# Optimization experiments

Hardware: AMD Instinct MI355X
Metric: run time of the kernel (lower is better)

The kernel has to match this reference:

```python
import jax, jax.numpy as jnp
import numpy as np

B, S, EMB, H = 4, 1024, 1024, 16
HD = EMB // H          # head_dim = 64
MAXP = 512             # RelativePositionalEncoder default max_position


def setup_inputs() -> dict:
    key = jax.random.key(0)
    ks = jax.random.split(key, 13)
    s = 1.0 / np.sqrt(EMB)  # xavier-ish scale keeps softmax logits sane
    return {
        "query": jax.random.normal(ks[0], (B, S, EMB), jnp.float32),
        "key": jax.random.normal(ks[1], (B, S, EMB), jnp.float32),
        "value": jax.random.normal(ks[2], (B, S, EMB), jnp.float32),
        "Wq": jax.random.normal(ks[3], (EMB, EMB), jnp.float32) * s,
        "bq": jnp.zeros((EMB,), jnp.float32),
        "Wk": jax.random.normal(ks[4], (EMB, EMB), jnp.float32) * s,
        "bk": jnp.zeros((EMB,), jnp.float32),
        "Wv": jax.random.normal(ks[5], (EMB, EMB), jnp.float32) * s,
        "bv": jnp.zeros((EMB,), jnp.float32),
        "Wo": jax.random.normal(ks[6], (EMB, EMB), jnp.float32) * s,
        "bo": jnp.zeros((EMB,), jnp.float32),
        "rel_k": jax.random.normal(ks[7], (2 * MAXP + 1, HD), jnp.float32) * 0.05,
        "rel_v": jax.random.normal(ks[8], (2 * MAXP + 1, HD), jnp.float32) * 0.05,
    }


def _split_heads(x):
    # [B,S,E] -> [B,S,H,HD] -> [B,H,S,HD] -> [B*H,S,HD]
    return x.reshape(B, S, H, HD).transpose(0, 2, 1, 3).reshape(B * H, S, HD)


def reference(query, key, value, Wq, bq, Wk, bk, Wv, bv, Wo, bo, rel_k, rel_v):
    scale = jnp.sqrt(jnp.asarray(HD, query.dtype))
    q = _split_heads(query @ Wq + bq)
    k = _split_heads(key @ Wk + bk)
    v = _split_heads(value @ Wv + bv)
    # relative position lookup tables: [Sq, Sk, HD]
    rp = jnp.clip(jnp.arange(S)[None, :] - jnp.arange(S)[:, None], -MAXP, MAXP) + MAXP
    a_key = rel_k[rp]
    a_value = rel_v[rp]
    qk = jnp.einsum('bqd,bkd->bqk', q, k)              # [B*H,S,S]
    rel_qk = jnp.einsum('bqd,qkd->bqk', q, a_key)      # relative score term
    attn = jax.nn.softmax((qk + rel_qk) / scale, axis=-1)
    out = jnp.einsum('bqk,bkd->bqd', attn, v) + jnp.einsum('bqk,qkd->bqd', attn, a_value)
    # faithful to original's view(num_heads, batch, -1, head_dim) then concat reshape
    out = out.reshape(H, B, S, HD).transpose(0, 2, 1, 3).reshape(B, S, H * HD)
    out = out @ Wo + bo
    return (out, attn)
```

## Files before the change

### kernel.cpp

```cpp
#include <hip/hip_runtime.h>


using s16x8 = __attribute__((ext_vector_type(8))) short;
using f32x4 = __attribute__((ext_vector_type(4))) float;

#define MFMA16 __builtin_amdgcn_mfma_f32_16x16x32_bf16

__device__ __forceinline__ float bf2f(unsigned short u) {
  union { unsigned int u; float f; } v; v.u = ((unsigned int)u) << 16; return v.f;
}
__device__ __forceinline__ unsigned short f2bf(float f) {
  union { float f; unsigned int u; } v; v.f = f;
  unsigned int r = (v.u + 0x7FFFu + ((v.u >> 16) & 1u)) >> 16;
  return (unsigned short)r;
}

__global__ void k_cvt_bf16(const float* __restrict__ in, unsigned short* __restrict__ out, int n) {
  int i = (blockIdx.x * 256 + threadIdx.x) * 8;
  if (i >= n) return;
  float4 a = *(const float4*)(in + i);
  float4 b = *(const float4*)(in + i + 4);
  s16x8 o;
  o[0] = (short)f2bf(a.x); o[1] = (short)f2bf(a.y); o[2] = (short)f2bf(a.z); o[3] = (short)f2bf(a.w);
  o[4] = (short)f2bf(b.x); o[5] = (short)f2bf(b.y); o[6] = (short)f2bf(b.z); o[7] = (short)f2bf(b.w);
  *(s16x8*)(out + i) = o;
}

__global__ void k_tr1024(const float* __restrict__ W, unsigned short* __restrict__ Wt) {
  __shared__ float t[32][33];
  int tx = threadIdx.x, ty = threadIdx.y;
  int n0 = blockIdx.x * 32, k0 = blockIdx.y * 32;
#pragma unroll
  for (int r = 0; r < 4; ++r)
    t[ty * 4 + r][tx] = W[(size_t)(k0 + ty * 4 + r) * 1024 + n0 + tx];
  __syncthreads();
#pragma unroll
  for (int r = 0; r < 4; ++r)
    Wt[(size_t)(n0 + ty * 4 + r) * 1024 + k0 + tx] = f2bf(t[tx][ty * 4 + r]);
}

__global__ void k_relprep(const float* __restrict__ rk, const float* __restrict__ rv,
                          unsigned short* __restrict__ relkb, unsigned short* __restrict__ rvTb) {
  int b = blockIdx.x;
  if (b < 33) {
    int i = (b * 256 + threadIdx.x) * 8;
    if (i < 65600) {
      float4 a = *(const float4*)(rk + i);
      float4 c = *(const float4*)(rk + i + 4);
      s16x8 o;
      o[0] = (short)f2bf(a.x); o[1] = (short)f2bf(a.y); o[2] = (short)f2bf(a.z); o[3] = (short)f2bf(a.w);
      o[4] = (short)f2bf(c.x); o[5] = (short)f2bf(c.y); o[6] = (short)f2bf(c.z); o[7] = (short)f2bf(c.w);
      *(s16x8*)(relkb + i) = o;
    }
  } else {
    int i = (b - 33) * 256 + threadIdx.x;
    if (i < 65600) {
      int p = i >> 6, d = i & 63;
      rvTb[d * 1040 + p] = f2bf(rv[i]);
    }
  }
}

__global__ __launch_bounds__(256)
void k_trV(const unsigned short* __restrict__ v, unsigned short* __restrict__ vt) {
  __shared__ unsigned short T[64][72];
  const int tid = threadIdx.x;
  const int bh = blockIdx.x >> 4;
  const int s0 = (blockIdx.x & 15) << 6;
  const int r = tid >> 2, cb = (tid & 3) << 4;
  const unsigned short* src = v + ((size_t)bh << 16) + (size_t)(s0 + r) * 64 + cb;
  *(s16x8*)&T[r][cb] = *(const s16x8*)src;
  *(s16x8*)&T[r][cb + 8] = *(const s16x8*)(src + 8);
  __syncthreads();
  unsigned short* dst = vt + ((size_t)bh << 16) + (size_t)r * 1024 + s0 + cb;
  s16x8 o0, o1;
#pragma unroll
  for (int e = 0; e < 8; ++e) o0[e] = T[cb + e][r];
#pragma unroll
  for (int e = 0; e < 8; ++e) o1[e] = T[cb + 8 + e][r];
  *(s16x8*)dst = o0;
  *(s16x8*)(dst + 8) = o1;
}

template <int MODE>
__global__ __launch_bounds__(256, 2)
void k_gemm(const unsigned short* __restrict__ A, const unsigned short* __restrict__ BT,
            const float* __restrict__ bias, void* __restrict__ Cout) {
  __shared__ alignas(16) unsigned short aT[2][4096];
  __shared__ alignas(16) unsigned short bT[2][4096];
  const int tid = threadIdx.x;
  const int lane = tid & 63;
  const int l15 = lane & 15, lhi = lane >> 4;
  const int w = tid >> 6;
  const int wr = (w >> 1) * 64, wc = (w & 1) * 64;
  const int brow = blockIdx.y * 128, bcol = blockIdx.x * 128;
  f32x4 acc[4][4] = {};

#define STAGE(buf, kt) do {                                                              \
    int k0s = (kt) * 32;                                                                 \
    {                                                                                    \
      int c = tid;                                                                       \
      int row = c >> 2, k8 = (c & 3) * 8;                                                \
      __builtin_amdgcn_global_load_lds(                                                  \
        (const __attribute__((address_space(1))) void*)(A + (size_t)(brow + row) * 1024 + k0s + k8), \
        (__attribute__((address_space(3))) void*)(&aT[buf][c * 8]), 16, 0, 0);           \
      __builtin_amdgcn_global_load_lds(                                                  \
        (const __attribute__((address_space(1))) void*)(BT + (size_t)(bcol + row) * 1024 + k0s + k8),\
        (__attribute__((address_space(3))) void*)(&bT[buf][c * 8]), 16, 0, 0);           \
    }                                                                                    \
    {                                                                                    \
      int c = tid + 256;                                                                 \
      int row = c >> 2, k8 = (c & 3) * 8;                                                \
      __builtin_amdgcn_global_load_lds(                                                  \
        (const __attribute__((address_space(1))) void*)(A + (size_t)(brow + row) * 1024 + k0s + k8), \
        (__attribute__((address_space(3))) void*)(&aT[buf][c * 8]), 16, 0, 0);           \
      __builtin_amdgcn_global_load_lds(                                                  \
        (const __attribute__((address_space(1))) void*)(BT + (size_t)(bcol + row) * 1024 + k0s + k8),\
        (__attribute__((address_space(3))) void*)(&bT[buf][c * 8]), 16, 0, 0);           \
    }                                                                                    \
  } while (0)

  int cur = 0;
  STAGE(0, 0);
  for (int kt = 0; kt < 32; ++kt) {
    __syncthreads();
    if (kt + 1 < 32) STAGE(cur ^ 1, kt + 1);
    s16x8 af[4], bfv[4];
#pragma unroll
    for (int m = 0; m < 4; ++m)
      af[m] = *(const s16x8*)&aT[cur][(wr + m * 16 + l15) * 32 + lhi * 8];
#pragma unroll
    for (int n = 0; n < 4; ++n)
      bfv[n] = *(const s16x8*)&bT[cur][(wc + n * 16 + l15) * 32 + lhi * 8];
#pragma unroll
    for (int m = 0; m < 4; ++m)
#pragma unroll
      for (int n = 0; n < 4; ++n)
        acc[m][n] = MFMA16(af[m], bfv[n], acc[m][n], 0, 0, 0);
    __syncthreads();
    cur ^= 1;
  }
#undef STAGE

#pragma unroll
  for (int m = 0; m < 4; ++m) {
#pragma unroll
    for (int n = 0; n < 4; ++n) {
      int col = bcol + wc + n * 16 + l15;
      float bs = bias[col];
#pragma unroll
      for (int j = 0; j < 4; ++j) {
        int r = brow + wr + m * 16 + lhi * 4 + j;
        float v = acc[m][n][j] + bs;
        if (MODE == 0) {
          int b = r >> 10, s = r & 1023, h = col >> 6, d = col & 63;
          ((unsigned short*)Cout)[(((size_t)((b << 4) + h) * 1024 + s) << 6) + d] = f2bf(v);
        } else {
          ((float*)Cout)[(size_t)r * 1024 + col] = v;
        }
      }
    }
  }
}

#define RPW 1032
#define PWP 520

__global__ __launch_bounds__(256, 3)
void k_attn(const unsigned short* __restrict__ qb, const unsigned short* __restrict__ kbm,
            const unsigned short* __restrict__ vT, const unsigned short* __restrict__ relk,
            const unsigned short* __restrict__ rvT, float* __restrict__ attn_out,
            unsigned short* __restrict__ xscr) {
  __shared__ alignas(16) unsigned short pbuf[16 * RPW];
  __shared__ alignas(16) unsigned short pw[16 * PWP];
  __shared__ float red[3][4][16];
  __shared__ float izS[16], plS[16], phS[16];

  const int tid = threadIdx.x;
  const int lane = tid & 63;
  const int w = tid >> 6;
  const int l15 = lane & 15, lhi = lane >> 4;
  const int bh = blockIdx.x >> 6;
  const int q0 = (blockIdx.x & 63) << 4;

  const unsigned short* Qh = qb + ((size_t)bh << 16);
  const unsigned short* Kh = kbm + ((size_t)bh << 16);
  const unsigned short* Vth = vT + ((size_t)bh << 16);

  const unsigned short* qp = Qh + (size_t)(q0 + l15) * 64 + lhi * 8;
  s16x8 qa0 = *(const s16x8*)qp;
  s16x8 qa1 = *(const s16x8*)(qp + 32);

  float zp[4] = {0.f, 0.f, 0.f, 0.f};
  float lo[4] = {0.f, 0.f, 0.f, 0.f};
  float hi4[4] = {0.f, 0.f, 0.f, 0.f};
  for (int k0 = w * 16; k0 < 1024; k0 += 64) {
    const unsigned short* kp = Kh + (size_t)(k0 + l15) * 64 + lhi * 8;
    s16x8 kf0 = *(const s16x8*)kp;
    s16x8 kf1 = *(const s16x8*)(kp + 32);
    const int jb = k0 - q0 - 15;
    int p0 = jb + l15;      p0 = (p0 < -512 ? -512 : (p0 > 512 ? 512 : p0)) + 512;
    int p1 = jb + l15 + 16; p1 = (p1 < -512 ? -512 : (p1 > 512 ? 512 : p1)) + 512;
    const unsigned short* r0p = relk + (size_t)p0 * 64 + lhi * 8;
    const unsigned short* r1p = relk + (size_t)p1 * 64 + lhi * 8;
    s16x8 ra0 = *(const s16x8*)r0p, ra0h = *(const s16x8*)(r0p + 32);
    s16x8 ra1 = *(const s16x8*)r1p, ra1h = *(const s16x8*)(r1p + 32);
    f32x4 c = {0.f, 0.f, 0.f, 0.f};
    f32x4 w0 = {0.f, 0.f, 0.f, 0.f}, w1 = {0.f, 0.f, 0.f, 0.f};
    __builtin_amdgcn_s_setprio(1);
    c = MFMA16(qa0, kf0, c, 0, 0, 0);
    c = MFMA16(qa1, kf1, c, 0, 0, 0);
    w0 = MFMA16(qa0, ra0, w0, 0, 0, 0);  w0 = MFMA16(qa1, ra0h, w0, 0, 0, 0);
    w1 = MFMA16(qa0, ra1, w1, 0, 0, 0);  w1 = MFMA16(qa1, ra1h, w1, 0, 0, 0);
    __builtin_amdgcn_s_setprio(0);
#pragma unroll
    for (int j = 0; j < 4; ++j) {
      int qi = lhi * 4 + j;
      int ts = l15 - qi + 15;
      int sl = (lane & 48) | (ts & 15);
      float a0 = __shfl(w0[j], sl, 64);
      float a1 = __shfl(w1[j], sl, 64);
      float rel = (ts & 16) ? a1 : a0;
      float e = __expf((c[j] + rel) * 0.125f);
      zp[j] += e;
      int dd = k0 + l15 - q0 - qi;
      lo[j]  += (dd <= -512) ? e : 0.f;
      hi4[j] += (dd >=  512) ? e : 0.f;
      pbuf[qi * RPW + k0 + l15] = f2bf(e);
    }
  }
#pragma unroll
  for (int off = 1; off < 16; off <<= 1)
#pragma unroll
    for (int j = 0; j < 4; ++j) {
      zp[j]  += __shfl_xor(zp[j], off, 64);
      lo[j]  += __shfl_xor(lo[j], off, 64);
      hi4[j] += __shfl_xor(hi4[j], off, 64);
    }
  if (l15 == 0) {
#pragma unroll
    for (int j = 0; j < 4; ++j) {
      red[0][w][lhi * 4 + j] = zp[j];
      red[1][w][lhi * 4 + j] = lo[j];
      red[2][w][lhi * 4 + j] = hi4[j];
    }
  }
  __syncthreads();
  if (tid < 16) {
    izS[tid] = 1.0f / (red[0][0][tid] + red[0][1][tid] + red[0][2][tid] + red[0][3][tid]);
    plS[tid] = red[1][0][tid] + red[1][1][tid] + red[1][2][tid] + red[1][3][tid];
    phS[tid] = red[2][0][tid] + red[2][1][tid] + red[2][2][tid] + red[2][3][tid];
  }
  __syncthreads();

  {
    float* ao = attn_out + ((size_t)bh << 20) + ((size_t)q0 << 10);
#pragma unroll
    for (int n = 0; n < 8; ++n) {
      int e8 = tid * 8 + n * 2048;
      int r = e8 >> 10, cc = e8 & 1023;
      float iz = izS[r];
      s16x8 p8 = *(const s16x8*)&pbuf[r * RPW + cc];
      f32x4 o0, o1;
      o0[0] = bf2f((unsigned short)p8[0]) * iz; o0[1] = bf2f((unsigned short)p8[1]) * iz;
      o0[2] = bf2f((unsigned short)p8[2]) * iz; o0[3] = bf2f((unsigned short)p8[3]) * iz;
      o1[0] = bf2f((unsigned short)p8[4]) * iz; o1[1] = bf2f((unsigned short)p8[5]) * iz;
      o1[2] = bf2f((unsigned short)p8[6]) * iz; o1[3] = bf2f((unsigned short)p8[7]) * iz;
      __builtin_nontemporal_store(o0, (f32x4*)(ao + e8));
      __builtin_nontemporal_store(o1, (f32x4*)(ao + e8 + 4));
    }
  }

  f32x4 acc = {0.f, 0.f, 0.f, 0.f};
  const int d0w = w << 4;
  const unsigned short* vrow = Vth + (size_t)(d0w + l15) * 1024 + lhi * 8;
#pragma unroll 8
  for (int kc = 0; kc < 1024; kc += 32) {
    s16x8 pa = *(const s16x8*)&pbuf[l15 * RPW + kc + lhi * 8];
    s16x8 vf = *(const s16x8*)(vrow + kc);
    acc = MFMA16(pa, vf, acc, 0, 0, 0);
  }

  const unsigned short* rrow = rvT + (size_t)(d0w + l15) * 1040 + lhi * 8;
  for (int ph = 0; ph < 2; ++ph) {
    __syncthreads();
    for (int n = 0; n < 32; ++n) {
      int e = n * 256 + tid;
      int qi = e >> 9, pp = e & 511;
      int p = (ph << 9) | pp;
      int k = q0 + qi + p - 512;
      unsigned short val;
      if (p == 0) val = f2bf(plS[qi]);
      else val = (k >= 0 && k < 1024) ? pbuf[qi * RPW + k] : (unsigned short)0;
      pw[qi * PWP + pp] = val;
    }
    __syncthreads();
#pragma unroll 8
    for (int kc = 0; kc < 512; kc += 32) {
      s16x8 pa = *(const s16x8*)&pw[l15 * PWP + kc + lhi * 8];
      s16x8 rb = *(const s16x8*)(rrow + (ph << 9) + kc);
      acc = MFMA16(pa, rb, acc, 0, 0, 0);
    }
  }

  float rv1024 = bf2f(rvT[(size_t)(d0w + l15) * 1040 + 1024]);
  const size_t fb = ((size_t)(bh >> 2) << 18) + ((size_t)(bh & 3) << 6);
#pragma unroll
  for (int j = 0; j < 4; ++j) {
    int qi = lhi * 4 + j;
    float v = (acc[j] + phS[qi] * rv1024) * izS[qi];
    xscr[fb + ((size_t)(q0 + qi) << 8) + d0w + l15] = f2bf(v);
  }
}

extern "C" void kernel_launch(void* const* d_in, const int* in_sizes, int n_in,
                              void* d_out, int out_size, void* d_ws, size_t ws_size,
                              hipStream_t stream) {
  (void)in_sizes; (void)n_in; (void)out_size; (void)ws_size;
  const float* query = (const float*)d_in[0];
  const float* key   = (const float*)d_in[1];
  const float* value = (const float*)d_in[2];
  const float* Wq = (const float*)d_in[3];
  const float* bq = (const float*)d_in[4];
  const float* Wk = (const float*)d_in[5];
  const float* bk = (const float*)d_in[6];
  const float* Wv = (const float*)d_in[7];
  const float* bv = (const float*)d_in[8];
  const float* Wo = (const float*)d_in[9];
  const float* bo = (const float*)d_in[10];
  const float* rel_k = (const float*)d_in[11];
  const float* rel_v = (const float*)d_in[12];

  char* ws = (char*)d_ws;
  const size_t MB = 1024 * 1024;
  unsigned short* qb    = (unsigned short*)(ws);
  unsigned short* kbuf  = (unsigned short*)(ws + 8 * MB);
  unsigned short* vbuf  = (unsigned short*)(ws + 16 * MB);
  unsigned short* tmp16 = (unsigned short*)(ws + 24 * MB);
  unsigned short* wt    = (unsigned short*)(ws + 32 * MB);
  unsigned short* relkb = (unsigned short*)(ws + 34 * MB);
  unsigned short* rvTb  = (unsigned short*)(ws + 34 * MB + 512 * 1024);
  unsigned short* vTb   = tmp16;
  unsigned short* xscr  = vbuf;

  float* out0 = (float*)d_out;
  float* attn_out = out0 + 4194304;

  dim3 trb(32, 8), trg(32, 32);
  dim3 gg(8, 32);

  k_relprep<<<290, 256, 0, stream>>>(rel_k, rel_v, relkb, rvTb);

  k_cvt_bf16<<<2048, 256, 0, stream>>>(query, tmp16, 4194304);
  k_tr1024<<<trg, trb, 0, stream>>>(Wq, wt);
  k_gemm<0><<<gg, 256, 0, stream>>>(tmp16, wt, bq, qb);

  k_cvt_bf16<<<2048, 256, 0, stream>>>(key, tmp16, 4194304);
  k_tr1024<<<trg, trb, 0, stream>>>(Wk, wt);
  k_gemm<0><<<gg, 256, 0, stream>>>(tmp16, wt, bk, kbuf);

  k_cvt_bf16<<<2048, 256, 0, stream>>>(value, tmp16, 4194304);
  k_tr1024<<<trg, trb, 0, stream>>>(Wv, wt);
  k_gemm<0><<<gg, 256, 0, stream>>>(tmp16, wt, bv, vbuf);

  k_trV<<<1024, 256, 0, stream>>>(vbuf, vTb);
  k_tr1024<<<trg, trb, 0, stream>>>(Wo, wt);

  k_attn<<<4096, 256, 0, stream>>>(qb, kbuf, vTb, relkb, rvTb, attn_out, xscr);

  k_gemm<1><<<gg, 256, 0, stream>>>(xscr, wt, bo, out0);
}
```

Before: 405.3 us.

## Retile projection GEMM, remap attention blocks, vectorize shifted P gather

```diff
diff --git a/kernel.cpp b/kernel.cpp
--- a/kernel.cpp
+++ b/kernel.cpp
@@ -87,14 +87,14 @@
 void k_gemm(const unsigned short* __restrict__ A, const unsigned short* __restrict__ BT,
             const float* __restrict__ bias, void* __restrict__ Cout) {
   __shared__ alignas(16) unsigned short aT[2][4096];
-  __shared__ alignas(16) unsigned short bT[2][4096];
+  __shared__ alignas(16) unsigned short bT[2][2048];
   const int tid = threadIdx.x;
   const int lane = tid & 63;
   const int l15 = lane & 15, lhi = lane >> 4;
   const int w = tid >> 6;
-  const int wr = (w >> 1) * 64, wc = (w & 1) * 64;
-  const int brow = blockIdx.y * 128, bcol = blockIdx.x * 128;
-  f32x4 acc[4][4] = {};
+  const int wr = w * 32;
+  const int brow = blockIdx.y * 128, bcol = blockIdx.x * 64;
+  f32x4 acc[2][4] = {};
 
 #define STAGE(buf, kt) do {                                                              \
     int k0s = (kt) * 32;                                                                 \
@@ -114,9 +114,6 @@
       __builtin_amdgcn_global_load_lds(                                                  \
         (const __attribute__((address_space(1))) void*)(A + (size_t)(brow + row) * 1024 + k0s + k8), \
         (__attribute__((address_space(3))) void*)(&aT[buf][c * 8]), 16, 0, 0);           \
-      __builtin_amdgcn_global_load_lds(                                                  \
-        (const __attribute__((address_space(1))) void*)(BT + (size_t)(bcol + row) * 1024 + k0s + k8),\
-        (__attribute__((address_space(3))) void*)(&bT[buf][c * 8]), 16, 0, 0);           \
     }                                                                                    \
   } while (0)
 
@@ -125,15 +122,15 @@
   for (int kt = 0; kt < 32; ++kt) {
     __syncthreads();
     if (kt + 1 < 32) STAGE(cur ^ 1, kt + 1);
-    s16x8 af[4], bfv[4];
-#pragma unroll
-    for (int m = 0; m < 4; ++m)
+    s16x8 af[2], bfv[4];
+#pragma unroll
+    for (int m = 0; m < 2; ++m)
       af[m] = *(const s16x8*)&aT[cur][(wr + m * 16 + l15) * 32 + lhi * 8];
 #pragma unroll
     for (int n = 0; n < 4; ++n)
-      bfv[n] = *(const s16x8*)&bT[cur][(wc + n * 16 + l15) * 32 + lhi * 8];
-#pragma unroll
-    for (int m = 0; m < 4; ++m)
+      bfv[n] = *(const s16x8*)&bT[cur][(n * 16 + l15) * 32 + lhi * 8];
+#pragma unroll
+    for (int m = 0; m < 2; ++m)
 #pragma unroll
       for (int n = 0; n < 4; ++n)
         acc[m][n] = MFMA16(af[m], bfv[n], acc[m][n], 0, 0, 0);
@@ -143,10 +140,10 @@
 #undef STAGE
 
 #pragma unroll
-  for (int m = 0; m < 4; ++m) {
+  for (int m = 0; m < 2; ++m) {
 #pragma unroll
     for (int n = 0; n < 4; ++n) {
-      int col = bcol + wc + n * 16 + l15;
+      int col = bcol + n * 16 + l15;
       float bs = bias[col];
 #pragma unroll
       for (int j = 0; j < 4; ++j) {
@@ -173,15 +170,16 @@
             unsigned short* __restrict__ xscr) {
   __shared__ alignas(16) unsigned short pbuf[16 * RPW];
   __shared__ alignas(16) unsigned short pw[16 * PWP];
-  __shared__ float red[3][4][16];
+  __shared__ float red[4][16];
   __shared__ float izS[16], plS[16], phS[16];
 
   const int tid = threadIdx.x;
   const int lane = tid & 63;
   const int w = tid >> 6;
   const int l15 = lane & 15, lhi = lane >> 4;
-  const int bh = blockIdx.x >> 6;
-  const int q0 = (blockIdx.x & 63) << 4;
+  const int orig = ((blockIdx.x & 7) << 9) | (blockIdx.x >> 3);
+  const int bh = orig >> 6;
+  const int q0 = (orig & 63) << 4;
 
   const unsigned short* Qh = qb + ((size_t)bh << 16);
   const unsigned short* Kh = kbm + ((size_t)bh << 16);
@@ -192,8 +190,6 @@
   s16x8 qa1 = *(const s16x8*)(qp + 32);
 
   float zp[4] = {0.f, 0.f, 0.f, 0.f};
-  float lo[4] = {0.f, 0.f, 0.f, 0.f};
-  float hi4[4] = {0.f, 0.f, 0.f, 0.f};
   for (int k0 = w * 16; k0 < 1024; k0 += 64) {
     const unsigned short* kp = Kh + (size_t)(k0 + l15) * 64 + lhi * 8;
     s16x8 kf0 = *(const s16x8*)kp;
@@ -223,51 +219,58 @@
       float rel = (ts & 16) ? a1 : a0;
       float e = __expf((c[j] + rel) * 0.125f);
       zp[j] += e;
-      int dd = k0 + l15 - q0 - qi;
-      lo[j]  += (dd <= -512) ? e : 0.f;
-      hi4[j] += (dd >=  512) ? e : 0.f;
       pbuf[qi * RPW + k0 + l15] = f2bf(e);
     }
   }
 #pragma unroll
   for (int off = 1; off < 16; off <<= 1)
 #pragma unroll
-    for (int j = 0; j < 4; ++j) {
-      zp[j]  += __shfl_xor(zp[j], off, 64);
-      lo[j]  += __shfl_xor(lo[j], off, 64);
-      hi4[j] += __shfl_xor(hi4[j], off, 64);
-    }
+    for (int j = 0; j < 4; ++j) zp[j] += __shfl_xor(zp[j], off, 64);
   if (l15 == 0) {
 #pragma unroll
-    for (int j = 0; j < 4; ++j) {
-      red[0][w][lhi * 4 + j] = zp[j];
-      red[1][w][lhi * 4 + j] = lo[j];
-      red[2][w][lhi * 4 + j] = hi4[j];
-    }
+    for (int j = 0; j < 4; ++j) red[w][lhi * 4 + j] = zp[j];
   }
   __syncthreads();
-  if (tid < 16) {
-    izS[tid] = 1.0f / (red[0][0][tid] + red[0][1][tid] + red[0][2][tid] + red[0][3][tid]);
-    plS[tid] = red[1][0][tid] + red[1][1][tid] + red[1][2][tid] + red[1][3][tid];
-    phS[tid] = red[2][0][tid] + red[2][1][tid] + red[2][2][tid] + red[2][3][tid];
+  if (tid < 16)
+    izS[tid] = 1.0f / (red[0][tid] + red[1][tid] + red[2][tid] + red[3][tid]);
+
+  {
+    const int qi = tid >> 4, tq = tid & 15;
+    const int qa = q0 + qi;
+    int lo, hi;
+    const bool isPh = (qa < 512);
+    if (isPh) { lo = qa + 512; hi = 1024; }
+    else      { lo = 0;        hi = qa - 511; }
+    float s = 0.f;
+    const unsigned short* srow = pbuf + qi * RPW;
+    const int kb0 = lo & ~7;
+    for (int k8 = kb0 + tq * 8; k8 < hi; k8 += 128) {
+      s16x8 v8 = *(const s16x8*)&srow[k8];
+#pragma unroll
+      for (int e = 0; e < 8; ++e) {
+        int k = k8 + e;
+        s += (k >= lo && k < hi) ? bf2f((unsigned short)v8[e]) : 0.f;
+      }
+    }
+#pragma unroll
+    for (int off = 1; off < 16; off <<= 1) s += __shfl_xor(s, off, 64);
+    if (tq == 0) { plS[qi] = isPh ? 0.f : s; phS[qi] = isPh ? s : 0.f; }
   }
   __syncthreads();
 
   {
     float* ao = attn_out + ((size_t)bh << 20) + ((size_t)q0 << 10);
 #pragma unroll
-    for (int n = 0; n < 8; ++n) {
-      int e8 = tid * 8 + n * 2048;
-      int r = e8 >> 10, cc = e8 & 1023;
-      float iz = izS[r];
-      s16x8 p8 = *(const s16x8*)&pbuf[r * RPW + cc];
-      f32x4 o0, o1;
-      o0[0] = bf2f((unsigned short)p8[0]) * iz; o0[1] = bf2f((unsigned short)p8[1]) * iz;
-      o0[2] = bf2f((unsigned short)p8[2]) * iz; o0[3] = bf2f((unsigned short)p8[3]) * iz;
-      o1[0] = bf2f((unsigned short)p8[4]) * iz; o1[1] = bf2f((unsigned short)p8[5]) * iz;
-      o1[2] = bf2f((unsigned short)p8[6]) * iz; o1[3] = bf2f((unsigned short)p8[7]) * iz;
-      __builtin_nontemporal_store(o0, (f32x4*)(ao + e8));
-      __builtin_nontemporal_store(o1, (f32x4*)(ao + e8 + 4));
+    for (int n = 0; n < 16; ++n) {
+      float iz = izS[n];
+      union { unsigned int u[2]; } pv;
+      *(uint2*)pv.u = *(const uint2*)&pbuf[n * RPW + tid * 4];
+      union { unsigned int u; float f; } b0, b1, b2, b3;
+      b0.u = pv.u[0] << 16; b1.u = pv.u[0] & 0xFFFF0000u;
+      b2.u = pv.u[1] << 16; b3.u = pv.u[1] & 0xFFFF0000u;
+      f32x4 o;
+      o[0] = b0.f * iz; o[1] = b1.f * iz; o[2] = b2.f * iz; o[3] = b3.f * iz;
+      __builtin_nontemporal_store(o, (f32x4*)(ao + (n << 10) + tid * 4));
     }
   }
 
@@ -282,24 +285,60 @@
   }
 
   const unsigned short* rrow = rvT + (size_t)(d0w + l15) * 1040 + lhi * 8;
-  for (int ph = 0; ph < 2; ++ph) {
-    __syncthreads();
-    for (int n = 0; n < 32; ++n) {
-      int e = n * 256 + tid;
-      int qi = e >> 9, pp = e & 511;
-      int p = (ph << 9) | pp;
-      int k = q0 + qi + p - 512;
-      unsigned short val;
-      if (p == 0) val = f2bf(plS[qi]);
-      else val = (k >= 0 && k < 1024) ? pbuf[qi * RPW + k] : (unsigned short)0;
-      pw[qi * PWP + pp] = val;
-    }
-    __syncthreads();
+  {
+    const int sqi = tid >> 4, stq = tid & 15;
+    const int ssh = sqi & 7, shs = ssh >> 1;
+    const bool sodd = (ssh & 1) != 0;
+    unsigned short* drow = pw + sqi * PWP;
+    const unsigned short* srow = pbuf + sqi * RPW;
+    for (int ph = 0; ph < 2; ++ph) {
+      __syncthreads();
+      const int base = q0 + sqi + (ph ? 0 : -512);
+      for (int t = stq; t < 64; t += 16) {
+        const int kw0 = base + t * 8;
+        s16x8 o;
+        if (kw0 >= 0 && kw0 + 8 <= 1024) {
+          const int A = kw0 - ssh;
+          union { s16x8 v; unsigned int u[4]; } a0, a1, ov;
+          a0.v = *(const s16x8*)&srow[A];
+          a1.v = *(const s16x8*)&srow[A + 8];
+          unsigned int wd[8];
+#pragma unroll
+          for (int j2 = 0; j2 < 4; ++j2) { wd[j2] = a0.u[j2]; wd[4 + j2] = a1.u[j2]; }
+          unsigned int v7[7];
+#pragma unroll
+          for (int j2 = 0; j2 < 7; ++j2) {
+            unsigned int sf = (wd[j2] >> 16) | (wd[j2 + 1] << 16);
+            v7[j2] = sodd ? sf : wd[j2];
+          }
+#pragma unroll
+          for (int j2 = 0; j2 < 4; ++j2) {
+            unsigned int t0 = (shs & 1) ? v7[j2 + 1] : v7[j2];
+            unsigned int t1 = (shs & 1) ? v7[j2 + 3] : v7[j2 + 2];
+            ov.u[j2] = (shs & 2) ? t1 : t0;
+          }
+          o = ov.v;
+        } else if (kw0 + 8 <= 0 || kw0 >= 1024) {
+          o = (s16x8){0, 0, 0, 0, 0, 0, 0, 0};
+        } else {
+#pragma unroll
+          for (int e = 0; e < 8; ++e) {
+            int k = kw0 + e;
+            int kc2 = k < 0 ? 0 : (k > 1023 ? 1023 : k);
+            unsigned short vv = srow[kc2];
+            o[e] = (k >= 0 && k < 1024) ? (short)vv : (short)0;
+          }
+        }
+        *(s16x8*)&drow[t * 8] = o;
+        if (ph == 0 && t == 0) drow[0] = f2bf(plS[sqi]);
+      }
+      __syncthreads();
 #pragma unroll 8
-    for (int kc = 0; kc < 512; kc += 32) {
-      s16x8 pa = *(const s16x8*)&pw[l15 * PWP + kc + lhi * 8];
-      s16x8 rb = *(const s16x8*)(rrow + (ph << 9) + kc);
-      acc = MFMA16(pa, rb, acc, 0, 0, 0);
+      for (int kc = 0; kc < 512; kc += 32) {
+        s16x8 pa = *(const s16x8*)&pw[l15 * PWP + kc + lhi * 8];
+        s16x8 rb = *(const s16x8*)(rrow + (ph << 9) + kc);
+        acc = MFMA16(pa, rb, acc, 0, 0, 0);
+      }
     }
   }
 
@@ -347,7 +386,7 @@
   float* attn_out = out0 + 4194304;
 
   dim3 trb(32, 8), trg(32, 32);
-  dim3 gg(8, 32);
+  dim3 gg(16, 32);
 
   k_relprep<<<290, 256, 0, stream>>>(rel_k, rel_v, relkb, rvTb);
 
```

New measurement: 395.8 us. 1.02x faster.
